# Optimization experiments

Measured on AMD Instinct MI355X. Metric: run time of the kernel, lower is better.

## Reference

```python
import jax, jax.numpy as jnp
import numpy as np

EMB = 128
BINS = 32
CUT = 5.0
NLAYER = 5
NHID = 4  # extra hidden linears in edge MLP (hidden_dim_list has 5 entries total)
N_NODES = 50000
N_EDGES = 800000
N_GRAPH = 256
NODE_CLASS = 100


def setup_inputs() -> dict:
    key = jax.random.key(0)
    ks = jax.random.split(key, 20)
    s = 0.02
    inp = {
        'z': jax.random.randint(ks[0], (N_NODES,), 0, NODE_CLASS),
        'pos': jax.random.normal(ks[1], (N_NODES, 3), dtype=jnp.float32) * 3.0,
        'batch': jnp.sort(jax.random.randint(ks[2], (N_NODES,), 0, N_GRAPH)),
        'edge_index': jax.random.randint(ks[3], (2, N_EDGES), 0, N_NODES),
        # parameters
        'atom_table': jax.random.normal(ks[4], (NODE_CLASS, EMB), dtype=jnp.float32) * s,
        'atom_w': jax.random.normal(ks[5], (EMB, EMB), dtype=jnp.float32) * s,
        'atom_b': jnp.zeros((EMB,), jnp.float32),
        'edge_emb_w': jax.random.normal(ks[6], (BINS, EMB), dtype=jnp.float32) * s,
        'edge_emb_b': jnp.zeros((EMB,), jnp.float32),
        'edge_w0': jax.random.normal(ks[7], (NLAYER, 3 * EMB, EMB), dtype=jnp.float32) * s,
        'edge_b0': jnp.zeros((NLAYER, EMB), jnp.float32),
        'edge_w': jax.random.normal(ks[8], (NLAYER, NHID, EMB, EMB), dtype=jnp.float32) * s,
        'edge_b': jnp.zeros((NLAYER, NHID, EMB), jnp.float32),
        'node_w': jax.random.normal(ks[9], (NLAYER, EMB, EMB), dtype=jnp.float32) * s,
        'node_b': jnp.zeros((NLAYER, EMB), jnp.float32),
        'out_w': jax.random.normal(ks[10], (EMB, 1), dtype=jnp.float32) * s,
        'out_b': jnp.zeros((1,), jnp.float32),
    }
    return inp


def reference(z, pos, batch, edge_index, atom_table, atom_w, atom_b,
              edge_emb_w, edge_emb_b, edge_w0, edge_b0, edge_w, edge_b,
              node_w, node_b, out_w, out_b):
    silu = jax.nn.silu
    row, col = edge_index[0], edge_index[1]

    # atom embedding + linear
    h_node = atom_table[z] @ atom_w + atom_b  # [N, EMB]

    # edge distances -> gaussian basis expansion (linear spacing, log_base=1.0)
    d = jnp.linalg.norm(pos[row] - pos[col], axis=-1)  # [E]
    mu = jnp.linspace(0.0, CUT, BINS, dtype=jnp.float32)
    sigma = CUT / BINS
    basis = jnp.exp(-0.5 * ((d[:, None] - mu) / sigma) ** 2)  # [E, BINS]
    h_edge = basis @ edge_emb_w + edge_emb_b  # [E, EMB]

    # message passing layers
    for l in range(NLAYER):
        m = jnp.concatenate([h_edge, h_node[row], h_node[col]], axis=-1)  # [E, 3*EMB]
        m = silu(m @ edge_w0[l] + edge_b0[l])
        for k in range(NHID):
            m = silu(m @ edge_w[l, k] + edge_b[l, k])
        h_edge = h_edge + m  # residual edge update
        agg = jax.ops.segment_sum(h_edge, row, num_segments=N_NODES)  # [N, EMB]
        h_node = h_node + silu(agg @ node_w[l] + node_b[l])  # residual node update

    # scatter-mean graph pool
    sums = jax.ops.segment_sum(h_node, batch, num_segments=N_GRAPH)
    cnt = jax.ops.segment_sum(jnp.ones((h_node.shape[0],), h_node.dtype), batch, num_segments=N_GRAPH)
    h_graph = sums / jnp.clip(cnt, 1.0)[:, None]

    return h_graph @ out_w + out_b  # [N_GRAPH, 1]
```

## Files before the change

### kernel.cpp

```cpp
#include <hip/hip_runtime.h>

#define EMB      128
#define N_NODES_ 50000
#define N_EDGES_ 800000
#define N_GRAPH_ 256
#define NLAYER_  5

typedef short short8 __attribute__((ext_vector_type(8)));
typedef float floatx4 __attribute__((ext_vector_type(4)));

__device__ __forceinline__ float silu_f(float x) {
    return __fdividef(x, 1.0f + __expf(-x));
}
__device__ __forceinline__ float bf2f(unsigned short h) {
    return __uint_as_float(((unsigned)h) << 16);
}
__device__ __forceinline__ unsigned short f2bf(float f) {
    unsigned u = __float_as_uint(f);
    unsigned r = 0x7FFFu + ((u >> 16) & 1u);
    return (unsigned short)((u + r) >> 16);
}

#if defined(__has_builtin)
#if __has_builtin(__builtin_amdgcn_cvt_pk_bf16_f32)
#define HAVE_PK_BF16 1
#endif
#endif
#ifdef HAVE_PK_BF16
typedef __bf16 bf16x2 __attribute__((ext_vector_type(2)));
__device__ __forceinline__ unsigned f2bf_pk(float a, float b) {
    bf16x2 v = __builtin_amdgcn_cvt_pk_bf16_f32(a, b);
    unsigned u;
    __builtin_memcpy(&u, &v, 4);
    return u;
}
#else
__device__ __forceinline__ unsigned f2bf_pk(float a, float b) {
    return (unsigned)f2bf(a) | ((unsigned)f2bf(b) << 16);
}
#endif

__global__ __launch_bounds__(256) void hist_kernel(
    const int* __restrict__ row, int* __restrict__ hist)
{
    const int e = blockIdx.x * 256 + threadIdx.x;
    if (e < N_EDGES_) atomicAdd(&hist[row[e]], 1);
}

__global__ __launch_bounds__(256) void scan_kernel(
    const int* __restrict__ hist, int* __restrict__ cursor)
{
    __shared__ int ssum[256];
    const int tid = threadIdx.x;
    const int chunk = (N_NODES_ + 255) / 256;
    const int base = tid * chunk;
    int s = 0;
    for (int i = 0; i < chunk; ++i) {
        const int idx = base + i;
        if (idx < N_NODES_) s += hist[idx];
    }
    ssum[tid] = s;
    __syncthreads();
    for (int off = 1; off < 256; off <<= 1) {
        const int t2 = (tid >= off) ? ssum[tid - off] : 0;
        __syncthreads();
        ssum[tid] += t2;
        __syncthreads();
    }
    int run = ssum[tid] - s;
    for (int i = 0; i < chunk; ++i) {
        const int idx = base + i;
        if (idx < N_NODES_) { cursor[idx] = run; run += hist[idx]; }
    }
}

__global__ __launch_bounds__(256) void scatter_kernel(
    const int* __restrict__ row, const int* __restrict__ col,
    int* __restrict__ cursor, int* __restrict__ row_s, int* __restrict__ col_s)
{
    const int e = blockIdx.x * 256 + threadIdx.x;
    if (e >= N_EDGES_) return;
    const int r = row[e];
    const int p = atomicAdd(&cursor[r], 1);
    row_s[p] = r;
    col_s[p] = col[e];
}

__global__ __launch_bounds__(256) void pack_w_kernel(
    const float* __restrict__ edge_w0, const float* __restrict__ edge_w,
    unsigned short* __restrict__ Wp)
{
    const int bid = blockIdx.x;
    const int l = bid / 40, r = bid % 40, s = r / 8, t = r % 8;
    const int Kb = (s == 0) ? 12 : 4;
    const float* __restrict__ src = (s == 0)
        ? edge_w0 + (size_t)l * 384 * 128
        : edge_w  + ((size_t)l * 4 + (s - 1)) * 128 * 128;
    unsigned short* __restrict__ dst =
        Wp + (size_t)l * 114688 + ((s == 0) ? 0 : (49152 + (s - 1) * 16384)) + (size_t)t * Kb * 512;
    const int n = Kb * 512;
    for (int p = threadIdx.x; p < n; p += 256) {
        const int j = p & 7, lane = (p >> 3) & 63, kb = p >> 9;
        const int k  = kb * 32 + ((lane >> 4) << 3) + j;
        const int nn = t * 16 + (lane & 15);
        dst[p] = f2bf(src[(size_t)k * 128 + nn]);
    }
}

__global__ __launch_bounds__(256, 3) void edge_mlp_sorted_kernel(
    const unsigned short* __restrict__ h_node_bf, unsigned short* __restrict__ h_edge,
    float* __restrict__ agg,
    const int* __restrict__ row_s, const int* __restrict__ col_s,
    const unsigned short* __restrict__ Wp,
    const float* __restrict__ b0, const float* __restrict__ bh)
{
    __shared__ __align__(16) unsigned short A[64][392];
    __shared__ int rv[64], cv[64];
    const int tid = threadIdx.x;
    const int e0 = blockIdx.x * 64;

    if (tid < 64) { rv[tid] = row_s[e0 + tid]; cv[tid] = col_s[e0 + tid]; }
    __syncthreads();

    {
        const int t = tid >> 2, q = tid & 3;
        const unsigned short* pe = &h_edge[(size_t)(e0 + t) * 128];
        const unsigned short* pr = &h_node_bf[(size_t)rv[t] * 128];
        const unsigned short* pc = &h_node_bf[(size_t)cv[t] * 128];
#pragma unroll
        for (int i = 0; i < 12; ++i) {
            const int ch = q + 4 * i;
            const int k8 = ch << 3;
            const unsigned short* src = (ch < 16) ? (pe + k8)
                                      : (ch < 32) ? (pr + (k8 - 128))
                                                  : (pc + (k8 - 256));
            *(short8*)&A[t][k8] = *(const short8*)src;
        }
    }
    __syncthreads();

    const int lane = tid & 63;
    const int wv   = tid >> 6;
    const int lr   = lane & 15;
    const int lg   = lane >> 4;
    const int nt0  = 2 * wv, nt1 = nt0 + 1;

    for (int s = 0; s < 5; ++s) {
        const int Kb = (s == 0) ? 12 : 4;
        const unsigned short* __restrict__ Ws =
            Wp + ((s == 0) ? 0 : (49152 + (s - 1) * 16384));
        const float* __restrict__ bias = (s == 0) ? b0 : (bh + (s - 1) * 128);

        const float4 bv0 = *(const float4*)&bias[nt0 * 16 + lg * 4];
        const float4 bv1 = *(const float4*)&bias[nt1 * 16 + lg * 4];
        floatx4 acc0[4], acc1[4];
#pragma unroll
        for (int et = 0; et < 4; ++et) {
            acc0[et] = (floatx4){bv0.x, bv0.y, bv0.z, bv0.w};
            acc1[et] = (floatx4){bv1.x, bv1.y, bv1.z, bv1.w};
        }

        const unsigned short* aptr0 = Ws + ((size_t)(nt0 * Kb) * 64 + lane) * 8;
        const unsigned short* aptr1 = Ws + ((size_t)(nt1 * Kb) * 64 + lane) * 8;
#pragma unroll 2
        for (int kb = 0; kb < Kb; ++kb) {
            const short8 wf0 = *(const short8*)(aptr0 + (size_t)kb * 512);
            const short8 wf1 = *(const short8*)(aptr1 + (size_t)kb * 512);
#pragma unroll
            for (int et = 0; et < 4; ++et) {
                const short8 mf = *(const short8*)&A[et * 16 + lr][kb * 32 + lg * 8];
                acc0[et] = __builtin_amdgcn_mfma_f32_16x16x32_bf16(wf0, mf, acc0[et], 0, 0, 0);
                acc1[et] = __builtin_amdgcn_mfma_f32_16x16x32_bf16(wf1, mf, acc1[et], 0, 0, 0);
            }
        }
        __syncthreads();
#pragma unroll
        for (int et = 0; et < 4; ++et) {
            uint2 p0, p1;
            p0.x = f2bf_pk(silu_f(acc0[et][0]), silu_f(acc0[et][1]));
            p0.y = f2bf_pk(silu_f(acc0[et][2]), silu_f(acc0[et][3]));
            p1.x = f2bf_pk(silu_f(acc1[et][0]), silu_f(acc1[et][1]));
            p1.y = f2bf_pk(silu_f(acc1[et][2]), silu_f(acc1[et][3]));
            *(uint2*)&A[et * 16 + lr][nt0 * 16 + lg * 4] = p0;
            *(uint2*)&A[et * 16 + lr][nt1 * 16 + lg * 4] = p1;
        }
        __syncthreads();
    }

    {
        const int t = tid >> 2, q = tid & 3;
        unsigned short* pe = &h_edge[(size_t)(e0 + t) * 128];
#pragma unroll
        for (int i = 0; i < 4; ++i) {
            const int k8 = (q + 4 * i) << 3;
            const short8 mv = *(const short8*)&A[t][k8];
            const short8 ov = *(const short8*)(pe + k8);
            float he[8];
#pragma unroll
            for (int j = 0; j < 8; ++j)
                he[j] = bf2f((unsigned short)ov[j]) + bf2f((unsigned short)mv[j]);
            uint4 sv;
            sv.x = f2bf_pk(he[0], he[1]);
            sv.y = f2bf_pk(he[2], he[3]);
            sv.z = f2bf_pk(he[4], he[5]);
            sv.w = f2bf_pk(he[6], he[7]);
            *(uint4*)(pe + k8) = sv;
            *(uint4*)&A[t][k8] = sv;
        }
    }
    __syncthreads();

    {
        const int c    = tid & 127;
        const int half = tid >> 7;
        const int tstart = half * 32;
        int curRow = rv[tstart];
        float accv = 0.f;
#pragma unroll 8
        for (int t = tstart; t < tstart + 32; ++t) {
            const int rr = rv[t];
            const float v = bf2f(A[t][c]);
            if (rr != curRow) {
                atomicAdd(&agg[(size_t)curRow * 128 + c], accv);
                accv = 0.f;
                curRow = rr;
            }
            accv += v;
        }
        atomicAdd(&agg[(size_t)curRow * 128 + c], accv);
    }
}

__device__ __forceinline__ void fma4x4(const float4 a[4], const float4& w0, const float4& w1,
                                       const float4& w2, const float4& w3, float acc[4][4]) {
#pragma unroll
    for (int i = 0; i < 4; ++i) {
        acc[i][0] = fmaf(a[i].x, w0.x, fmaf(a[i].y, w1.x, fmaf(a[i].z, w2.x, fmaf(a[i].w, w3.x, acc[i][0]))));
        acc[i][1] = fmaf(a[i].x, w0.y, fmaf(a[i].y, w1.y, fmaf(a[i].z, w2.y, fmaf(a[i].w, w3.y, acc[i][1]))));
        acc[i][2] = fmaf(a[i].x, w0.z, fmaf(a[i].y, w1.z, fmaf(a[i].z, w2.z, fmaf(a[i].w, w3.z, acc[i][2]))));
        acc[i][3] = fmaf(a[i].x, w0.w, fmaf(a[i].y, w1.w, fmaf(a[i].z, w2.w, fmaf(a[i].w, w3.w, acc[i][3]))));
    }
}

template <int GATHER, int RESID, int SILU>
__global__ __launch_bounds__(256, 4) void row_gemm_bf_kernel(
    const float* __restrict__ src, const int* __restrict__ gidx,
    const float* __restrict__ W, const float* __restrict__ bias,
    unsigned short* __restrict__ dst, int N)
{
    __shared__ __align__(16) float A[32][132];
    const int tid = threadIdx.x;
    const int n0 = blockIdx.x * 32;

    for (int idx = tid; idx < 32 * 32; idx += 256) {
        int t = idx >> 5, k = (idx & 31) << 2;
        int n = n0 + t;
        float4 v = make_float4(0.f, 0.f, 0.f, 0.f);
        if (n < N) {
            int rr = GATHER ? gidx[n] : n;
            v = *(const float4*)&src[(size_t)rr * 128 + k];
        }
        *(float4*)&A[t][k] = v;
    }
    __syncthreads();

    const int r = tid >> 5, c = tid & 31;
    const int t0 = r << 2, j0 = c << 2;
    float acc[4][4] = {{0.f, 0.f, 0.f, 0.f}};
#pragma unroll 2
    for (int kk = 0; kk < 128; kk += 4) {
        float4 a[4];
#pragma unroll
        for (int i = 0; i < 4; ++i) a[i] = *(const float4*)&A[t0 + i][kk];
        const float4 w0 = *(const float4*)&W[(size_t)(kk + 0) * 128 + j0];
        const float4 w1 = *(const float4*)&W[(size_t)(kk + 1) * 128 + j0];
        const float4 w2 = *(const float4*)&W[(size_t)(kk + 2) * 128 + j0];
        const float4 w3 = *(const float4*)&W[(size_t)(kk + 3) * 128 + j0];
        fma4x4(a, w0, w1, w2, w3, acc);
    }
    const float4 bv = *(const float4*)&bias[j0];
    const float bias4[4] = {bv.x, bv.y, bv.z, bv.w};
#pragma unroll
    for (int i = 0; i < 4; ++i) {
        int n = n0 + t0 + i;
        if (n >= N) continue;
        float x[4];
#pragma unroll
        for (int jj = 0; jj < 4; ++jj) {
            x[jj] = acc[i][jj] + bias4[jj];
            if (SILU) x[jj] = silu_f(x[jj]);
        }
        const size_t off = (size_t)n * 128 + j0;
        if (RESID) {
            const ushort4 d = *(const ushort4*)&dst[off];
            x[0] += bf2f(d.x); x[1] += bf2f(d.y); x[2] += bf2f(d.z); x[3] += bf2f(d.w);
        }
        uint2 p;
        p.x = f2bf_pk(x[0], x[1]);
        p.y = f2bf_pk(x[2], x[3]);
        *(uint2*)&dst[off] = p;
    }
}

__global__ __launch_bounds__(256) void edge_embed_kernel(
    const float* __restrict__ pos, const int* __restrict__ row, const int* __restrict__ col,
    const float* __restrict__ Wemb, const float* __restrict__ bemb,
    unsigned short* __restrict__ h_edge, int E)
{
    __shared__ __align__(16) float Ws[32][128];
    __shared__ float bas[8][32];
    const int tid = threadIdx.x;
    {
        const float4* Wv = (const float4*)Wemb;
        float4* Wsv = (float4*)Ws;
        for (int idx = tid; idx < 1024; idx += 256) Wsv[idx] = Wv[idx];
    }
    const int g = tid >> 5, k = tid & 31;
    const int j = tid & 127, gh = tid >> 7;
    const float mu   = (float)k * (5.0f / 31.0f);
    const float invs = 32.0f / 5.0f;

    for (int eb = blockIdx.x * 8; eb < E; eb += gridDim.x * 8) {
        __syncthreads();
        const int e = eb + g;
        const int rr = row[e], cc = col[e];
        const float dx = pos[rr * 3 + 0] - pos[cc * 3 + 0];
        const float dy = pos[rr * 3 + 1] - pos[cc * 3 + 1];
        const float dz = pos[rr * 3 + 2] - pos[cc * 3 + 2];
        const float d = sqrtf(dx * dx + dy * dy + dz * dz);
        const float t = (d - mu) * invs;
        bas[g][k] = __expf(-0.5f * t * t);
        __syncthreads();
#pragma unroll
        for (int gg = 0; gg < 4; ++gg) {
            const int ge = (gh << 2) + gg;
            float h = bemb[j];
#pragma unroll
            for (int kk = 0; kk < 32; ++kk) h = fmaf(bas[ge][kk], Ws[kk][j], h);
            h_edge[(size_t)(eb + ge) * 128 + j] = f2bf(h);
        }
    }
}

__global__ __launch_bounds__(128) void pool_kernel(
    const unsigned short* __restrict__ h_node_bf, const int* __restrict__ batch,
    float* __restrict__ sums, float* __restrict__ cnt, int N)
{
    __shared__ int bb[256];
    const int tid = threadIdx.x;
    const int n0 = blockIdx.x * 256;
    for (int idx = tid; idx < 256; idx += 128) {
        int n = n0 + idx;
        bb[idx] = (n < N) ? batch[n] : -1;
    }
    __syncthreads();
    int cur = bb[0];
    float run = 0.f, runc = 0.f;
    for (int i = 0; i < 256; ++i) {
        const int b = bb[i];
        if (b < 0) break;
        if (b != cur) {
            atomicAdd(&sums[(size_t)cur * 128 + tid], run);
            if (tid == 0) atomicAdd(&cnt[cur], runc);
            run = 0.f; runc = 0.f; cur = b;
        }
        run += bf2f(h_node_bf[(size_t)(n0 + i) * 128 + tid]);
        runc += 1.f;
    }
    atomicAdd(&sums[(size_t)cur * 128 + tid], run);
    if (tid == 0) atomicAdd(&cnt[cur], runc);
}

__global__ __launch_bounds__(256) void final_kernel(
    const float* __restrict__ sums, const float* __restrict__ cnt,
    const float* __restrict__ out_w, const float* __restrict__ out_b,
    float* __restrict__ out)
{
    const int g = threadIdx.x;
    const float c = fmaxf(cnt[g], 1.0f);
    float acc = 0.f;
    for (int jj = 0; jj < 128; ++jj) acc = fmaf(sums[(size_t)g * 128 + jj], out_w[jj], acc);
    out[g] = acc / c + out_b[0];
}

__global__ void zero_out_kernel(float* out, int n) {
    int i = blockIdx.x * 256 + threadIdx.x;
    if (i < n) out[i] = 0.f;
}


extern "C" void kernel_launch(void* const* d_in, const int* in_sizes, int n_in,
                              void* d_out, int out_size, void* d_ws, size_t ws_size,
                              hipStream_t stream)
{
    const int*   z          = (const int*)  d_in[0];
    const float* pos        = (const float*)d_in[1];
    const int*   batch      = (const int*)  d_in[2];
    const int*   eidx       = (const int*)  d_in[3];
    const float* atom_table = (const float*)d_in[4];
    const float* atom_w     = (const float*)d_in[5];
    const float* atom_b     = (const float*)d_in[6];
    const float* edge_emb_w = (const float*)d_in[7];
    const float* edge_emb_b = (const float*)d_in[8];
    const float* edge_w0    = (const float*)d_in[9];
    const float* edge_b0    = (const float*)d_in[10];
    const float* edge_w     = (const float*)d_in[11];
    const float* edge_b     = (const float*)d_in[12];
    const float* node_w     = (const float*)d_in[13];
    const float* node_b     = (const float*)d_in[14];
    const float* out_w      = (const float*)d_in[15];
    const float* out_b      = (const float*)d_in[16];
    const int* row = eidx;
    const int* col = eidx + N_EDGES_;

    float* aggb = (float*)d_ws;
    float* sums = aggb + (size_t)N_NODES_ * EMB;
    float* cnt  = sums + (size_t)N_GRAPH_ * EMB;
    unsigned short* h_node_bf = (unsigned short*)(cnt + N_GRAPH_);
    unsigned short* h_edge    = h_node_bf + (size_t)N_NODES_ * EMB;
    unsigned short* Wp        = h_edge + (size_t)N_EDGES_ * EMB;
    int* hist   = (int*)(Wp + (size_t)NLAYER_ * 114688);
    int* cursor = hist + N_NODES_;
    int* row_s  = cursor + N_NODES_;
    int* col_s  = row_s + N_EDGES_;

    const size_t need = ((size_t)(N_NODES_ * EMB + N_GRAPH_ * EMB + N_GRAPH_)) * 4
                      + ((size_t)N_NODES_ * EMB + (size_t)N_EDGES_ * EMB + (size_t)NLAYER_ * 114688) * 2
                      + ((size_t)N_NODES_ * 2 + (size_t)N_EDGES_ * 2) * 4;

    if (ws_size < need) {
        zero_out_kernel<<<1, 256, 0, stream>>>((float*)d_out, N_GRAPH_);
        return;
    }

    const int grid_rows = (N_NODES_ + 31) / 32;

    (void)hipMemsetAsync(hist, 0, N_NODES_ * sizeof(int), stream);
    hist_kernel<<<(N_EDGES_ + 255) / 256, 256, 0, stream>>>(row, hist);
    scan_kernel<<<1, 256, 0, stream>>>(hist, cursor);
    scatter_kernel<<<(N_EDGES_ + 255) / 256, 256, 0, stream>>>(row, col, cursor, row_s, col_s);

    row_gemm_bf_kernel<1, 0, 0><<<grid_rows, 256, 0, stream>>>(
        atom_table, z, atom_w, atom_b, h_node_bf, N_NODES_);
    edge_embed_kernel<<<1024, 256, 0, stream>>>(pos, row_s, col_s, edge_emb_w, edge_emb_b, h_edge, N_EDGES_);
    pack_w_kernel<<<200, 256, 0, stream>>>(edge_w0, edge_w, Wp);

    for (int l = 0; l < NLAYER_; ++l) {
        (void)hipMemsetAsync(aggb, 0, (size_t)N_NODES_ * EMB * sizeof(float), stream);
        edge_mlp_sorted_kernel<<<N_EDGES_ / 64, 256, 0, stream>>>(
            h_node_bf, h_edge, aggb, row_s, col_s,
            Wp + (size_t)l * 114688,
            edge_b0 + (size_t)l * 128, edge_b + (size_t)l * 4 * 128);
        row_gemm_bf_kernel<0, 1, 1><<<grid_rows, 256, 0, stream>>>(
            aggb, nullptr, node_w + (size_t)l * 128 * 128, node_b + (size_t)l * 128,
            h_node_bf, N_NODES_);
    }

    (void)hipMemsetAsync(sums, 0, ((size_t)N_GRAPH_ * EMB + N_GRAPH_) * sizeof(float), stream);
    pool_kernel<<<(N_NODES_ + 255) / 256, 128, 0, stream>>>(h_node_bf, batch, sums, cnt, N_NODES_);
    final_kernel<<<1, 256, 0, stream>>>(sums, cnt, out_w, out_b, (float*)d_out);
}
```

Measured before the change: 2.998 ms.

## Move node GEMMs and edge embedding to MFMA, make edge MLP wave-private

The node-update and atom-embedding GEMMs, along with the edge basis embedding, now run on bf16 MFMA. Their weights are pre-packed in the same layout as the edge MLP weights, replacing the scalar FP32 FMA paths. The edge MLP is restructured so each wave owns 16 edge rows and all 128 output columns. This replaces block-wide __syncthreads with wave-level fences, but each wave now reloads every weight fragment from global or L2 memory. Node inputs are rounded to bf16 before the GEMM, which adds some precision loss.

```diff
diff --git a/kernel.cpp b/kernel.cpp
--- a/kernel.cpp
+++ b/kernel.cpp
@@ -5,6 +5,11 @@
 #define N_EDGES_ 800000
 #define N_GRAPH_ 256
 #define NLAYER_  5
+
+#define WP_ATOM  573440
+#define WP_NODE0 589824
+#define WP_EMB   671744
+#define WP_TOTAL 675840
 
 typedef short short8 __attribute__((ext_vector_type(8)));
 typedef float floatx4 __attribute__((ext_vector_type(4)));
@@ -40,6 +45,11 @@
 }
 #endif
 
+__device__ __forceinline__ void wave_lds_fence() {
+    __builtin_amdgcn_fence(__ATOMIC_ACQ_REL, "wavefront");
+    __builtin_amdgcn_wave_barrier();
+}
+
 __global__ __launch_bounds__(256) void hist_kernel(
     const int* __restrict__ row, int* __restrict__ hist)
 {
@@ -88,16 +98,33 @@
 
 __global__ __launch_bounds__(256) void pack_w_kernel(
     const float* __restrict__ edge_w0, const float* __restrict__ edge_w,
+    const float* __restrict__ atom_w, const float* __restrict__ node_w,
+    const float* __restrict__ edge_emb_w,
     unsigned short* __restrict__ Wp)
 {
     const int bid = blockIdx.x;
-    const int l = bid / 40, r = bid % 40, s = r / 8, t = r % 8;
-    const int Kb = (s == 0) ? 12 : 4;
-    const float* __restrict__ src = (s == 0)
-        ? edge_w0 + (size_t)l * 384 * 128
-        : edge_w  + ((size_t)l * 4 + (s - 1)) * 128 * 128;
-    unsigned short* __restrict__ dst =
-        Wp + (size_t)l * 114688 + ((s == 0) ? 0 : (49152 + (s - 1) * 16384)) + (size_t)t * Kb * 512;
+    int Kb, t;
+    const float* src;
+    unsigned short* dst;
+    if (bid < 200) {
+        const int l = bid / 40, r = bid % 40, s = r / 8;
+        t = r % 8;
+        Kb = (s == 0) ? 12 : 4;
+        src = (s == 0) ? edge_w0 + (size_t)l * 384 * 128
+                       : edge_w + ((size_t)l * 4 + (s - 1)) * 128 * 128;
+        dst = Wp + (size_t)l * 114688 + ((s == 0) ? 0 : (49152 + (s - 1) * 16384))
+            + (size_t)t * Kb * 512;
+    } else if (bid < 208) {
+        t = bid - 200; Kb = 4; src = atom_w;
+        dst = Wp + WP_ATOM + (size_t)t * Kb * 512;
+    } else if (bid < 248) {
+        const int l = (bid - 208) >> 3; t = (bid - 208) & 7; Kb = 4;
+        src = node_w + (size_t)l * 128 * 128;
+        dst = Wp + WP_NODE0 + (size_t)l * 16384 + (size_t)t * Kb * 512;
+    } else {
+        t = bid - 248; Kb = 1; src = edge_emb_w;
+        dst = Wp + WP_EMB + (size_t)t * 512;
+    }
     const int n = Kb * 512;
     for (int p = threadIdx.x; p < n; p += 256) {
         const int j = p & 7, lane = (p >> 3) & 63, kb = p >> 9;
@@ -107,7 +134,7 @@
     }
 }
 
-__global__ __launch_bounds__(256, 3) void edge_mlp_sorted_kernel(
+__global__ __launch_bounds__(256, 3) void edge_mlp_wp_kernel(
     const unsigned short* __restrict__ h_node_bf, unsigned short* __restrict__ h_edge,
     float* __restrict__ agg,
     const int* __restrict__ row_s, const int* __restrict__ col_s,
@@ -115,18 +142,21 @@
     const float* __restrict__ b0, const float* __restrict__ bh)
 {
     __shared__ __align__(16) unsigned short A[64][392];
-    __shared__ int rv[64], cv[64];
-    const int tid = threadIdx.x;
-    const int e0 = blockIdx.x * 64;
-
-    if (tid < 64) { rv[tid] = row_s[e0 + tid]; cv[tid] = col_s[e0 + tid]; }
-    __syncthreads();
+    __shared__ int rv[64];
+    const int tid  = threadIdx.x;
+    const int lane = tid & 63;
+    const int wv   = tid >> 6;
+    const int e0   = blockIdx.x * 64;
+
+    if (lane < 16) rv[wv * 16 + lane] = row_s[e0 + wv * 16 + lane];
 
     {
         const int t = tid >> 2, q = tid & 3;
+        const int rg = row_s[e0 + t];
+        const int cg = col_s[e0 + t];
         const unsigned short* pe = &h_edge[(size_t)(e0 + t) * 128];
-        const unsigned short* pr = &h_node_bf[(size_t)rv[t] * 128];
-        const unsigned short* pc = &h_node_bf[(size_t)cv[t] * 128];
+        const unsigned short* pr = &h_node_bf[(size_t)rg * 128];
+        const unsigned short* pc = &h_node_bf[(size_t)cg * 128];
 #pragma unroll
         for (int i = 0; i < 12; ++i) {
             const int ch = q + 4 * i;
@@ -137,13 +167,11 @@
             *(short8*)&A[t][k8] = *(const short8*)src;
         }
     }
-    __syncthreads();
-
-    const int lane = tid & 63;
-    const int wv   = tid >> 6;
-    const int lr   = lane & 15;
-    const int lg   = lane >> 4;
-    const int nt0  = 2 * wv, nt1 = nt0 + 1;
+    wave_lds_fence();
+
+    const int lr = lane & 15;
+    const int lg = lane >> 4;
+    unsigned short* myrow = &A[wv * 16 + lr][0];
 
     for (int s = 0; s < 5; ++s) {
         const int Kb = (s == 0) ? 12 : 4;
@@ -151,40 +179,30 @@
             Wp + ((s == 0) ? 0 : (49152 + (s - 1) * 16384));
         const float* __restrict__ bias = (s == 0) ? b0 : (bh + (s - 1) * 128);
 
-        const float4 bv0 = *(const float4*)&bias[nt0 * 16 + lg * 4];
-        const float4 bv1 = *(const float4*)&bias[nt1 * 16 + lg * 4];
-        floatx4 acc0[4], acc1[4];
-#pragma unroll
-        for (int et = 0; et < 4; ++et) {
-            acc0[et] = (floatx4){bv0.x, bv0.y, bv0.z, bv0.w};
-            acc1[et] = (floatx4){bv1.x, bv1.y, bv1.z, bv1.w};
-        }
-
-        const unsigned short* aptr0 = Ws + ((size_t)(nt0 * Kb) * 64 + lane) * 8;
-        const unsigned short* aptr1 = Ws + ((size_t)(nt1 * Kb) * 64 + lane) * 8;
+        floatx4 acc[8];
+#pragma unroll
+        for (int nt = 0; nt < 8; ++nt) {
+            const float4 bv = *(const float4*)&bias[nt * 16 + lg * 4];
+            acc[nt] = (floatx4){bv.x, bv.y, bv.z, bv.w};
+        }
 #pragma unroll 2
         for (int kb = 0; kb < Kb; ++kb) {
-            const short8 wf0 = *(const short8*)(aptr0 + (size_t)kb * 512);
-            const short8 wf1 = *(const short8*)(aptr1 + (size_t)kb * 512);
-#pragma unroll
-            for (int et = 0; et < 4; ++et) {
-                const short8 mf = *(const short8*)&A[et * 16 + lr][kb * 32 + lg * 8];
-                acc0[et] = __builtin_amdgcn_mfma_f32_16x16x32_bf16(wf0, mf, acc0[et], 0, 0, 0);
-                acc1[et] = __builtin_amdgcn_mfma_f32_16x16x32_bf16(wf1, mf, acc1[et], 0, 0, 0);
+            const short8 mf = *(const short8*)(myrow + kb * 32 + lg * 8);
+#pragma unroll
+            for (int nt = 0; nt < 8; ++nt) {
+                const short8 wf = *(const short8*)(Ws + ((size_t)(nt * Kb + kb) * 64 + lane) * 8);
+                acc[nt] = __builtin_amdgcn_mfma_f32_16x16x32_bf16(wf, mf, acc[nt], 0, 0, 0);
             }
         }
-        __syncthreads();
-#pragma unroll
-        for (int et = 0; et < 4; ++et) {
-            uint2 p0, p1;
-            p0.x = f2bf_pk(silu_f(acc0[et][0]), silu_f(acc0[et][1]));
-            p0.y = f2bf_pk(silu_f(acc0[et][2]), silu_f(acc0[et][3]));
-            p1.x = f2bf_pk(silu_f(acc1[et][0]), silu_f(acc1[et][1]));
-            p1.y = f2bf_pk(silu_f(acc1[et][2]), silu_f(acc1[et][3]));
-            *(uint2*)&A[et * 16 + lr][nt0 * 16 + lg * 4] = p0;
-            *(uint2*)&A[et * 16 + lr][nt1 * 16 + lg * 4] = p1;
-        }
-        __syncthreads();
+        wave_lds_fence();
+#pragma unroll
+        for (int nt = 0; nt < 8; ++nt) {
+            uint2 p;
+            p.x = f2bf_pk(silu_f(acc[nt][0]), silu_f(acc[nt][1]));
+            p.y = f2bf_pk(silu_f(acc[nt][2]), silu_f(acc[nt][3]));
+            *(uint2*)(myrow + nt * 16 + lg * 4) = p;
+        }
+        wave_lds_fence();
     }
 
     {
@@ -231,114 +249,138 @@
     }
 }
 
-__device__ __forceinline__ void fma4x4(const float4 a[4], const float4& w0, const float4& w1,
-                                       const float4& w2, const float4& w3, float acc[4][4]) {
-#pragma unroll
-    for (int i = 0; i < 4; ++i) {
-        acc[i][0] = fmaf(a[i].x, w0.x, fmaf(a[i].y, w1.x, fmaf(a[i].z, w2.x, fmaf(a[i].w, w3.x, acc[i][0]))));
-        acc[i][1] = fmaf(a[i].x, w0.y, fmaf(a[i].y, w1.y, fmaf(a[i].z, w2.y, fmaf(a[i].w, w3.y, acc[i][1]))));
-        acc[i][2] = fmaf(a[i].x, w0.z, fmaf(a[i].y, w1.z, fmaf(a[i].z, w2.z, fmaf(a[i].w, w3.z, acc[i][2]))));
-        acc[i][3] = fmaf(a[i].x, w0.w, fmaf(a[i].y, w1.w, fmaf(a[i].z, w2.w, fmaf(a[i].w, w3.w, acc[i][3]))));
-    }
-}
-
 template <int GATHER, int RESID, int SILU>
-__global__ __launch_bounds__(256, 4) void row_gemm_bf_kernel(
+__global__ __launch_bounds__(256, 4) void row_gemm_mfma_kernel(
     const float* __restrict__ src, const int* __restrict__ gidx,
-    const float* __restrict__ W, const float* __restrict__ bias,
+    const unsigned short* __restrict__ Wpm, const float* __restrict__ bias,
     unsigned short* __restrict__ dst, int N)
 {
-    __shared__ __align__(16) float A[32][132];
-    const int tid = threadIdx.x;
-    const int n0 = blockIdx.x * 32;
-
-    for (int idx = tid; idx < 32 * 32; idx += 256) {
-        int t = idx >> 5, k = (idx & 31) << 2;
-        int n = n0 + t;
-        float4 v = make_float4(0.f, 0.f, 0.f, 0.f);
-        if (n < N) {
-            int rr = GATHER ? gidx[n] : n;
-            v = *(const float4*)&src[(size_t)rr * 128 + k];
-        }
-        *(float4*)&A[t][k] = v;
-    }
-    __syncthreads();
-
-    const int r = tid >> 5, c = tid & 31;
-    const int t0 = r << 2, j0 = c << 2;
-    float acc[4][4] = {{0.f, 0.f, 0.f, 0.f}};
+    __shared__ __align__(16) unsigned short B[64][136];
+    const int tid  = threadIdx.x;
+    const int lane = tid & 63;
+    const int wv   = tid >> 6;
+    const int n0   = blockIdx.x * 64;
+
+    {
+        const int t = tid >> 2, q = tid & 3;
+        const int node = n0 + t;
+        const float* srow = src;
+        if (node < N) {
+            const int rr = GATHER ? gidx[node] : node;
+            srow = &src[(size_t)rr * 128];
+        }
+#pragma unroll
+        for (int i = 0; i < 4; ++i) {
+            const int k8 = (q + 4 * i) << 3;
+            uint4 pk = make_uint4(0, 0, 0, 0);
+            if (node < N) {
+                const float4 f0 = *(const float4*)(srow + k8);
+                const float4 f1 = *(const float4*)(srow + k8 + 4);
+                pk.x = f2bf_pk(f0.x, f0.y);
+                pk.y = f2bf_pk(f0.z, f0.w);
+                pk.z = f2bf_pk(f1.x, f1.y);
+                pk.w = f2bf_pk(f1.z, f1.w);
+            }
+            *(uint4*)&B[t][k8] = pk;
+        }
+    }
+    wave_lds_fence();
+
+    const int lr = lane & 15, lg = lane >> 4;
+    floatx4 acc[8];
+#pragma unroll
+    for (int nt = 0; nt < 8; ++nt) {
+        const float4 bv = *(const float4*)&bias[nt * 16 + lg * 4];
+        acc[nt] = (floatx4){bv.x, bv.y, bv.z, bv.w};
+    }
+    const unsigned short* brow = &B[wv * 16 + lr][0];
 #pragma unroll 2
-    for (int kk = 0; kk < 128; kk += 4) {
-        float4 a[4];
-#pragma unroll
-        for (int i = 0; i < 4; ++i) a[i] = *(const float4*)&A[t0 + i][kk];
-        const float4 w0 = *(const float4*)&W[(size_t)(kk + 0) * 128 + j0];
-        const float4 w1 = *(const float4*)&W[(size_t)(kk + 1) * 128 + j0];
-        const float4 w2 = *(const float4*)&W[(size_t)(kk + 2) * 128 + j0];
-        const float4 w3 = *(const float4*)&W[(size_t)(kk + 3) * 128 + j0];
-        fma4x4(a, w0, w1, w2, w3, acc);
-    }
-    const float4 bv = *(const float4*)&bias[j0];
-    const float bias4[4] = {bv.x, bv.y, bv.z, bv.w};
-#pragma unroll
-    for (int i = 0; i < 4; ++i) {
-        int n = n0 + t0 + i;
-        if (n >= N) continue;
-        float x[4];
-#pragma unroll
-        for (int jj = 0; jj < 4; ++jj) {
-            x[jj] = acc[i][jj] + bias4[jj];
-            if (SILU) x[jj] = silu_f(x[jj]);
-        }
-        const size_t off = (size_t)n * 128 + j0;
-        if (RESID) {
-            const ushort4 d = *(const ushort4*)&dst[off];
-            x[0] += bf2f(d.x); x[1] += bf2f(d.y); x[2] += bf2f(d.z); x[3] += bf2f(d.w);
-        }
-        uint2 p;
-        p.x = f2bf_pk(x[0], x[1]);
-        p.y = f2bf_pk(x[2], x[3]);
-        *(uint2*)&dst[off] = p;
-    }
-}
-
-__global__ __launch_bounds__(256) void edge_embed_kernel(
+    for (int kb = 0; kb < 4; ++kb) {
+        const short8 mf = *(const short8*)(brow + kb * 32 + lg * 8);
+#pragma unroll
+        for (int nt = 0; nt < 8; ++nt) {
+            const short8 wf = *(const short8*)(Wpm + ((size_t)(nt * 4 + kb) * 64 + lane) * 8);
+            acc[nt] = __builtin_amdgcn_mfma_f32_16x16x32_bf16(wf, mf, acc[nt], 0, 0, 0);
+        }
+    }
+    const int node = n0 + wv * 16 + lr;
+    if (node < N) {
+        unsigned short* drow = &dst[(size_t)node * 128];
+#pragma unroll
+        for (int nt = 0; nt < 8; ++nt) {
+            float x0 = acc[nt][0], x1 = acc[nt][1], x2 = acc[nt][2], x3 = acc[nt][3];
+            if (SILU) { x0 = silu_f(x0); x1 = silu_f(x1); x2 = silu_f(x2); x3 = silu_f(x3); }
+            unsigned short* p = drow + nt * 16 + lg * 4;
+            if (RESID) {
+                const uint2 d = *(const uint2*)p;
+                x0 += bf2f((unsigned short)(d.x & 0xFFFF));
+                x1 += bf2f((unsigned short)(d.x >> 16));
+                x2 += bf2f((unsigned short)(d.y & 0xFFFF));
+                x3 += bf2f((unsigned short)(d.y >> 16));
+            }
+            uint2 o;
+            o.x = f2bf_pk(x0, x1);
+            o.y = f2bf_pk(x2, x3);
+            *(uint2*)p = o;
+        }
+    }
+}
+
+__global__ __launch_bounds__(256, 4) void edge_embed_mfma_kernel(
     const float* __restrict__ pos, const int* __restrict__ row, const int* __restrict__ col,
-    const float* __restrict__ Wemb, const float* __restrict__ bemb,
-    unsigned short* __restrict__ h_edge, int E)
-{
-    __shared__ __align__(16) float Ws[32][128];
-    __shared__ float bas[8][32];
-    const int tid = threadIdx.x;
+    const unsigned short* __restrict__ Wpe, const float* __restrict__ bemb,
+    unsigned short* __restrict__ h_edge)
+{
+    __shared__ __align__(16) unsigned short Bas[64][40];
+    const int tid  = threadIdx.x;
+    const int lane = tid & 63;
+    const int wv   = tid >> 6;
+    const int e0   = blockIdx.x * 64;
+
     {
-        const float4* Wv = (const float4*)Wemb;
-        float4* Wsv = (float4*)Ws;
-        for (int idx = tid; idx < 1024; idx += 256) Wsv[idx] = Wv[idx];
-    }
-    const int g = tid >> 5, k = tid & 31;
-    const int j = tid & 127, gh = tid >> 7;
-    const float mu   = (float)k * (5.0f / 31.0f);
-    const float invs = 32.0f / 5.0f;
-
-    for (int eb = blockIdx.x * 8; eb < E; eb += gridDim.x * 8) {
-        __syncthreads();
-        const int e = eb + g;
-        const int rr = row[e], cc = col[e];
+        const int t = tid >> 2, q = tid & 3;
+        const int rr = row[e0 + t], cc = col[e0 + t];
         const float dx = pos[rr * 3 + 0] - pos[cc * 3 + 0];
         const float dy = pos[rr * 3 + 1] - pos[cc * 3 + 1];
         const float dz = pos[rr * 3 + 2] - pos[cc * 3 + 2];
         const float d = sqrtf(dx * dx + dy * dy + dz * dz);
-        const float t = (d - mu) * invs;
-        bas[g][k] = __expf(-0.5f * t * t);
-        __syncthreads();
-#pragma unroll
-        for (int gg = 0; gg < 4; ++gg) {
-            const int ge = (gh << 2) + gg;
-            float h = bemb[j];
-#pragma unroll
-            for (int kk = 0; kk < 32; ++kk) h = fmaf(bas[ge][kk], Ws[kk][j], h);
-            h_edge[(size_t)(eb + ge) * 128 + j] = f2bf(h);
-        }
+        const float invs = 32.0f / 5.0f;
+        float e[8];
+#pragma unroll
+        for (int j = 0; j < 8; ++j) {
+            const float mu = (float)(q * 8 + j) * (5.0f / 31.0f);
+            const float tt = (d - mu) * invs;
+            e[j] = __expf(-0.5f * tt * tt);
+        }
+        uint4 pk;
+        pk.x = f2bf_pk(e[0], e[1]);
+        pk.y = f2bf_pk(e[2], e[3]);
+        pk.z = f2bf_pk(e[4], e[5]);
+        pk.w = f2bf_pk(e[6], e[7]);
+        *(uint4*)&Bas[t][q * 8] = pk;
+    }
+    wave_lds_fence();
+
+    const int lr = lane & 15, lg = lane >> 4;
+    floatx4 acc[8];
+#pragma unroll
+    for (int nt = 0; nt < 8; ++nt) {
+        const float4 bv = *(const float4*)&bemb[nt * 16 + lg * 4];
+        acc[nt] = (floatx4){bv.x, bv.y, bv.z, bv.w};
+    }
+    const short8 mf = *(const short8*)&Bas[wv * 16 + lr][lg * 8];
+#pragma unroll
+    for (int nt = 0; nt < 8; ++nt) {
+        const short8 wf = *(const short8*)(Wpe + ((size_t)nt * 64 + lane) * 8);
+        acc[nt] = __builtin_amdgcn_mfma_f32_16x16x32_bf16(wf, mf, acc[nt], 0, 0, 0);
+    }
+    unsigned short* erow = &h_edge[(size_t)(e0 + wv * 16 + lr) * 128];
+#pragma unroll
+    for (int nt = 0; nt < 8; ++nt) {
+        uint2 o;
+        o.x = f2bf_pk(acc[nt][0], acc[nt][1]);
+        o.y = f2bf_pk(acc[nt][2], acc[nt][3]);
+        *(uint2*)(erow + nt * 16 + lg * 4) = o;
     }
 }
 
@@ -419,13 +461,13 @@
     unsigned short* h_node_bf = (unsigned short*)(cnt + N_GRAPH_);
     unsigned short* h_edge    = h_node_bf + (size_t)N_NODES_ * EMB;
     unsigned short* Wp        = h_edge + (size_t)N_EDGES_ * EMB;
-    int* hist   = (int*)(Wp + (size_t)NLAYER_ * 114688);
+    int* hist   = (int*)(Wp + WP_TOTAL);
     int* cursor = hist + N_NODES_;
     int* row_s  = cursor + N_NODES_;
     int* col_s  = row_s + N_EDGES_;
 
     const size_t need = ((size_t)(N_NODES_ * EMB + N_GRAPH_ * EMB + N_GRAPH_)) * 4
-                      + ((size_t)N_NODES_ * EMB + (size_t)N_EDGES_ * EMB + (size_t)NLAYER_ * 114688) * 2
+                      + ((size_t)N_NODES_ * EMB + (size_t)N_EDGES_ * EMB + (size_t)WP_TOTAL) * 2
                       + ((size_t)N_NODES_ * 2 + (size_t)N_EDGES_ * 2) * 4;
 
     if (ws_size < need) {
@@ -433,26 +475,28 @@
         return;
     }
 
-    const int grid_rows = (N_NODES_ + 31) / 32;
+    const int grid_rows64 = (N_NODES_ + 63) / 64;
 
     (void)hipMemsetAsync(hist, 0, N_NODES_ * sizeof(int), stream);
     hist_kernel<<<(N_EDGES_ + 255) / 256, 256, 0, stream>>>(row, hist);
     scan_kernel<<<1, 256, 0, stream>>>(hist, cursor);
     scatter_kernel<<<(N_EDGES_ + 255) / 256, 256, 0, stream>>>(row, col, cursor, row_s, col_s);
 
-    row_gemm_bf_kernel<1, 0, 0><<<grid_rows, 256, 0, stream>>>(
-        atom_table, z, atom_w, atom_b, h_node_bf, N_NODES_);
-    edge_embed_kernel<<<1024, 256, 0, stream>>>(pos, row_s, col_s, edge_emb_w, edge_emb_b, h_edge, N_EDGES_);
-    pack_w_kernel<<<200, 256, 0, stream>>>(edge_w0, edge_w, Wp);
+    pack_w_kernel<<<256, 256, 0, stream>>>(edge_w0, edge_w, atom_w, node_w, edge_emb_w, Wp);
+
+    row_gemm_mfma_kernel<1, 0, 0><<<grid_rows64, 256, 0, stream>>>(
+        atom_table, z, Wp + WP_ATOM, atom_b, h_node_bf, N_NODES_);
+    edge_embed_mfma_kernel<<<N_EDGES_ / 64, 256, 0, stream>>>(
+        pos, row_s, col_s, Wp + WP_EMB, edge_emb_b, h_edge);
 
     for (int l = 0; l < NLAYER_; ++l) {
         (void)hipMemsetAsync(aggb, 0, (size_t)N_NODES_ * EMB * sizeof(float), stream);
-        edge_mlp_sorted_kernel<<<N_EDGES_ / 64, 256, 0, stream>>>(
+        edge_mlp_wp_kernel<<<N_EDGES_ / 64, 256, 0, stream>>>(
             h_node_bf, h_edge, aggb, row_s, col_s,
             Wp + (size_t)l * 114688,
             edge_b0 + (size_t)l * 128, edge_b + (size_t)l * 4 * 128);
-        row_gemm_bf_kernel<0, 1, 1><<<grid_rows, 256, 0, stream>>>(
-            aggb, nullptr, node_w + (size_t)l * 128 * 128, node_b + (size_t)l * 128,
+        row_gemm_mfma_kernel<0, 1, 1><<<grid_rows64, 256, 0, stream>>>(
+            aggb, nullptr, Wp + WP_NODE0 + (size_t)l * 16384, node_b + (size_t)l * 128,
             h_node_bf, N_NODES_);
     }
 
```

New measurement: 3.932 ms. 31.2% more time.
